# Kernel tuning notes

Hardware: AMD Instinct MI355X
Metric: run time of the kernel (lower is better)

The kernel has to match this reference:

```python
import jax, jax.numpy as jnp
import numpy as np

PAGE_SIZE = 16
NUM_PAGES = 256
H = 32          # query heads
HKV = 8         # kv heads
D = 128         # head dim
HIDDEN = 4096
SEQ = 2048
ROPE_THETA = 10000.0


def _rope(x, pos):
    # x: [S, h, D], pos: [S]; non-interleaved (rotate-half) RoPE as in
    # flashinfer.rope.apply_rope_pos_ids_inplace / HF Llama.
    half = x.shape[-1] // 2
    inv_freq = 1.0 / (ROPE_THETA ** (jnp.arange(half, dtype=jnp.float32) / half))
    ang = pos.astype(jnp.float32)[:, None] * inv_freq          # [S, half]
    cos = jnp.cos(ang)[:, None, :]
    sin = jnp.sin(ang)[:, None, :]
    x1, x2 = x[..., :half], x[..., half:]
    return jnp.concatenate([x1 * cos - x2 * sin, x2 * cos + x1 * sin], axis=-1).astype(x.dtype)


def setup_inputs() -> dict:
    key = jax.random.key(0)
    ks = jax.random.split(key, 6)
    return {
        "hidden_states": jax.random.normal(ks[0], (1, SEQ, HIDDEN), jnp.float32),
        "position_ids": jnp.arange(SEQ, dtype=jnp.int32),
        "page_indices": jnp.arange(SEQ // PAGE_SIZE, dtype=jnp.int32),  # 128 distinct pages
        "Wq": jax.random.normal(ks[1], (H * D, HIDDEN), jnp.float32) * 0.02,
        "Wk": jax.random.normal(ks[2], (HKV * D, HIDDEN), jnp.float32) * 0.02,
        "Wv": jax.random.normal(ks[3], (HKV * D, HIDDEN), jnp.float32) * 0.02,
        "Wo": jax.random.normal(ks[4], (HIDDEN, H * D), jnp.float32) * 0.02,
        "kv_cache": jnp.zeros((NUM_PAGES, 2, PAGE_SIZE, HKV, D), jnp.float32),
    }


def reference(hidden_states, position_ids, page_indices, Wq, Wk, Wv, Wo, kv_cache):
    S = hidden_states.shape[1]
    x = hidden_states[0]                                  # [S, HIDDEN] (module squeezes batch=1)
    q = (x @ Wq.T).reshape(S, H, D)
    k = (x @ Wk.T).reshape(S, HKV, D)
    v = (x @ Wv.T).reshape(S, HKV, D)
    q = _rope(q, position_ids)
    k = _rope(k, position_ids)

    # Write K/V into the paged cache (page_table.write_block per page)
    n_used = page_indices.shape[0]
    k_pages = k.reshape(n_used, PAGE_SIZE, HKV, D)
    v_pages = v.reshape(n_used, PAGE_SIZE, HKV, D)
    cache = kv_cache.at[page_indices, 0].set(k_pages).at[page_indices, 1].set(v_pages)

    # Gather paged KV back for attention (BatchPrefillWithPagedKVCache)
    kk = cache[page_indices, 0].reshape(-1, HKV, D)[:S]   # [S, HKV, D]
    vv = cache[page_indices, 1].reshape(-1, HKV, D)[:S]

    # GQA: expand kv heads to query heads
    group = H // HKV
    k_rep = jnp.repeat(kk, group, axis=1)                 # [S, H, D]
    v_rep = jnp.repeat(vv, group, axis=1)

    scale = D ** -0.5
    scores = jnp.einsum('qhd,khd->hqk', q * scale, k_rep)  # [H, S, S]
    causal = jnp.arange(S)[:, None] >= jnp.arange(S)[None, :]
    scores = jnp.where(causal[None], scores, jnp.finfo(scores.dtype).min)
    probs = jax.nn.softmax(scores, axis=-1)
    attn = jnp.einsum('hqk,khd->qhd', probs, v_rep)        # [S, H, D]

    out = attn.reshape(S, H * D) @ Wo.T                    # o_proj
    return out[None]                                       # [1, S, HIDDEN]
```

## Files before the change

kernel.cpp:

```cpp
#include <hip/hip_runtime.h>
#include <hip/hip_bf16.h>
#include <math.h>

#define SEQ    2048
#define HIDDEN 4096
#define NH     32
#define NKV    8
#define HD     128
#define QKV_N  6144

typedef __attribute__((ext_vector_type(8))) short bf16x8;
typedef __attribute__((ext_vector_type(4))) float f32x4;
typedef unsigned short u16;
typedef unsigned int u32;

#define VMCNT(n) asm volatile("s_waitcnt vmcnt(" #n ")" ::: "memory")

__device__ inline void gl_lds16(const void* g, void* lds) {
  __builtin_amdgcn_global_load_lds((const __attribute__((address_space(1))) void*)g,
                                   (__attribute__((address_space(3))) void*)lds, 16, 0, 0);
}

__device__ inline void tile_barrier() {
  __builtin_amdgcn_sched_barrier(0);
  __builtin_amdgcn_s_barrier();
  __builtin_amdgcn_sched_barrier(0);
}

__device__ inline u16 f2bf(float f) {
  __hip_bfloat16 h = __float2bfloat16(f);
  return *(u16*)&h;
}
__device__ inline float bf2f(u16 u) {
  __hip_bfloat16 h = *(__hip_bfloat16*)&u;
  return __bfloat162float(h);
}

__global__ void cvt_f32_bf16(const float* __restrict__ src, u16* __restrict__ dst, int n8) {
  int i = blockIdx.x * blockDim.x + threadIdx.x;
  if (i >= n8) return;
  const float4* s = (const float4*)src + (size_t)i * 2;
  float4 a = s[0], b = s[1];
  float v[8] = {a.x, a.y, a.z, a.w, b.x, b.y, b.z, b.w};
  union { u16 o[8]; uint4 u; } pk;
#pragma unroll
  for (int j = 0; j < 8; j++) pk.o[j] = f2bf(v[j]);
  *(uint4*)(dst + (size_t)i * 8) = pk.u;
}

template <int OUTF32, int NF>
__global__ __launch_bounds__(512, 2) void gemm_bt2(const u16* __restrict__ A,
                                                   const u16* __restrict__ B,
                                                   void* __restrict__ Cout,
                                                   int M, int N, int K) {
  __shared__ __align__(16) u16 Abuf[4][256 * 32];
  __shared__ __align__(16) u16 Bbuf[4][NF * 64 * 32];
  const int tid = threadIdx.x;
  const int w = tid >> 6, lane = tid & 63;
  const int quad = lane >> 4, l16 = lane & 15;
  const int wm = w >> 2, wn = w & 3;
  constexpr int BN = NF * 64;

  const int nwg = gridDim.x;
  const int bid = blockIdx.x;
  const int qq = nwg >> 3, rr8 = nwg & 7;
  const int xcd = bid & 7, loc = bid >> 3;
  const int wg = (xcd < rr8 ? xcd * (qq + 1) : rr8 * (qq + 1) + (xcd - rr8) * qq) + loc;
  const int nbx = N / BN;
  const int m0 = (wg / nbx) * 256;
  const int n0 = (wg % nbx) * BN;

  const int srow = lane >> 2;
  const int sswz = ((lane >> 2) & 3) ^ ((lane >> 4) & 1);
  const int scol = ((lane & 3) ^ sswz) << 3;
  const u16* aG = A + (size_t)(m0 + w * 16 + srow) * K + scol;
  const u16* bG = B + (size_t)(n0 + w * 16 + srow) * K + scol;
  const int NT = K >> 5;

  const int swzr = (l16 & 3) ^ ((l16 >> 2) & 1);
  const int kslot = (quad ^ swzr) << 3;

  f32x4 acc[8][NF] = {};

  auto stage = [&](int t) {
    const int b = t & 3;
    const size_t k0 = (size_t)t << 5;
    gl_lds16(aG + k0,                   &Abuf[b][(w * 16) * 32]);
    gl_lds16(aG + k0 + (size_t)128 * K, &Abuf[b][(128 + w * 16) * 32]);
    gl_lds16(bG + k0,                   &Bbuf[b][(w * 16) * 32]);
    if constexpr (NF == 4)
      gl_lds16(bG + k0 + (size_t)128 * K, &Bbuf[b][(128 + w * 16) * 32]);
  };

  stage(0); stage(1); stage(2);
  if constexpr (NF == 4) { VMCNT(8); } else { VMCNT(6); }
  tile_barrier();

  for (int t = 0; t < NT; ++t) {
    const int b = t & 3;
    if (t + 3 < NT) stage(t + 3);

    bf16x8 af[8], bfr[NF];
#pragma unroll
    for (int f = 0; f < 8; ++f)
      af[f] = *(const bf16x8*)&Abuf[b][(wm * 128 + f * 16 + l16) * 32 + kslot];
#pragma unroll
    for (int nf = 0; nf < NF; ++nf)
      bfr[nf] = *(const bf16x8*)&Bbuf[b][(wn * (NF * 16) + nf * 16 + l16) * 32 + kslot];

    __builtin_amdgcn_s_setprio(1);
#pragma unroll
    for (int f = 0; f < 8; ++f)
#pragma unroll
      for (int nf = 0; nf < NF; ++nf)
        acc[f][nf] = __builtin_amdgcn_mfma_f32_16x16x32_bf16(af[f], bfr[nf], acc[f][nf], 0, 0, 0);
    __builtin_amdgcn_s_setprio(0);

    if (t < NT - 1) {
      if (t + 3 < NT) {
        if constexpr (NF == 4) { VMCNT(8); } else { VMCNT(6); }
      } else if (t + 3 == NT) {
        if constexpr (NF == 4) { VMCNT(4); } else { VMCNT(3); }
      } else {
        VMCNT(0);
      }
      tile_barrier();
    }
  }

#pragma unroll
  for (int f = 0; f < 8; ++f)
#pragma unroll
    for (int nf = 0; nf < NF; ++nf)
#pragma unroll
      for (int r = 0; r < 4; ++r) {
        int row = m0 + wm * 128 + f * 16 + quad * 4 + r;
        int col = n0 + wn * (NF * 16) + nf * 16 + l16;
        float v = acc[f][nf][r];
        if (OUTF32) ((float*)Cout)[(size_t)row * N + col] = v;
        else        ((u16*)Cout)[(size_t)row * N + col] = f2bf(v);
      }
}

__global__ void rope_kernel(u16* __restrict__ qkv, const int* __restrict__ pos_ids) {
  int idx = blockIdx.x * blockDim.x + threadIdx.x;
  int d = idx & 63;
  int h = (idx >> 6) % 40;
  int s = idx / (64 * 40);
  if (s >= SEQ) return;
  int off = (h < NH) ? h * HD : HIDDEN + (h - NH) * HD;
  u16* base = qkv + (size_t)s * QKV_N + off;
  float inv_freq = powf(10000.0f, -(float)d * (1.0f / 64.0f));
  float ang = (float)pos_ids[s] * inv_freq;
  float sn, cs;
  sincosf(ang, &sn, &cs);
  float x1 = bf2f(base[d]);
  float x2 = bf2f(base[d + 64]);
  base[d]      = f2bf(x1 * cs - x2 * sn);
  base[d + 64] = f2bf(x2 * cs + x1 * sn);
}

__global__ __launch_bounds__(256) void transpose_v(const u16* __restrict__ qkv,
                                                   u16* __restrict__ vt) {
  __shared__ u16 t[64][72];
  const int s0 = blockIdx.x * 64, c0 = blockIdx.y * 64;
  const int tid = threadIdx.x;
#pragma unroll
  for (int i = 0; i < 2; i++) {
    int r = (tid >> 3) + i * 32;
    int c = (tid & 7) * 8;
    *(uint4*)&t[r][c] = *(const uint4*)&qkv[(size_t)(s0 + r) * QKV_N + 5120 + c0 + c];
  }
  __syncthreads();
#pragma unroll
  for (int i = 0; i < 2; i++) {
    int c = (tid >> 3) + i * 32;
    int s = (tid & 7) * 8;
    union { uint4 u; u16 e[8]; } o;
#pragma unroll
    for (int j = 0; j < 8; j++) o.e[j] = t[s + j][c];
    *(uint4*)&vt[(size_t)(c0 + c) * SEQ + s0 + s] = o.u;
  }
}

__global__ __launch_bounds__(128, 3) void attn_kernel(const u16* __restrict__ qkv,
                                                      const u16* __restrict__ vt,
                                                      u16* __restrict__ attn_out) {
  __shared__ __align__(16) float Ex[32 * 132];
  const int blk = blockIdx.x;
  const int kvh = blk & 7;
  const int hg = (blk >> 3) & 3;
  const int it = 63 - (blk >> 5);
  const int h  = kvh * 4 + hg;
  const int tid = threadIdx.x;
  const int wave = tid >> 6, lane = tid & 63;
  const int quad = lane >> 4, l16 = lane & 15;
  const int q0 = it * 32;

  const float c = 0.08838834764831845f * 1.4426950408889634f;

  bf16x8 qf[2][4];
#pragma unroll
  for (int m = 0; m < 2; m++)
#pragma unroll
    for (int dc = 0; dc < 4; dc++)
      qf[m][dc] = *(const bf16x8*)(qkv + (size_t)(q0 + m * 16 + l16) * QKV_N + h * HD + dc * 32 + quad * 8);

  const u16* kp[4];
#pragma unroll
  for (int st = 0; st < 4; st++)
    kp[st] = qkv + (size_t)(wave * 64 + st * 16 + l16) * QKV_N + HIDDEN + kvh * HD + quad * 8;
  const u16* vp[8];
#pragma unroll
  for (int dt = 0; dt < 8; dt++)
    vp[dt] = vt + (size_t)(kvh * HD + dt * 16 + l16) * SEQ + wave * 64 + quad * 8;

  float lsum[2] = {0.f, 0.f};
  f32x4 o[2][8] = {};

  const int srcA = ((lane >> 4) & 1) * 32 + l16;
  const int srcB = srcA + 16;
  const bool hi = quad >= 2;

  const int n_kt = (q0 + 95) >> 6;
  for (int kt = wave; kt < n_kt; kt += 2) {
    const bool last = (kt == n_kt - 1);

    u32 pk[2][4][2];
#pragma unroll
    for (int st = 0; st < 4; st++) {
      bf16x8 kst[4];
#pragma unroll
      for (int dc = 0; dc < 4; dc++) kst[dc] = *(const bf16x8*)(kp[st] + dc * 32);
      f32x4 s[2] = {};
#pragma unroll
      for (int dc = 0; dc < 4; dc++)
#pragma unroll
        for (int m = 0; m < 2; m++)
          s[m] = __builtin_amdgcn_mfma_f32_16x16x32_bf16(kst[dc], qf[m][dc], s[m], 0, 0, 0);
#pragma unroll
      for (int m = 0; m < 2; m++) {
        float pr[4];
#pragma unroll
        for (int r = 0; r < 4; r++) {
          float v = fmaf(s[m][r], c, -32.0f);
          if (last) {
            int key = kt * 64 + st * 16 + quad * 4 + r;
            if (key > q0 + m * 16 + l16) v = -1e30f;
          }
          pr[r] = exp2f(v);
          lsum[m] += pr[r];
        }
        pk[m][st][0] = ((u32)f2bf(pr[1]) << 16) | f2bf(pr[0]);
        pk[m][st][1] = ((u32)f2bf(pr[3]) << 16) | f2bf(pr[2]);
      }
    }

    bf16x8 pf[2][2];
#pragma unroll
    for (int m = 0; m < 2; m++)
#pragma unroll
      for (int kc = 0; kc < 2; kc++) {
        union { u32 w[4]; bf16x8 v; } u;
        u32 a0 = (u32)__shfl((int)pk[m][2 * kc][0],     srcA);
        u32 b0 = (u32)__shfl((int)pk[m][2 * kc + 1][0], srcA);
        u32 a1 = (u32)__shfl((int)pk[m][2 * kc][1],     srcA);
        u32 b1 = (u32)__shfl((int)pk[m][2 * kc + 1][1], srcA);
        u32 a2 = (u32)__shfl((int)pk[m][2 * kc][0],     srcB);
        u32 b2 = (u32)__shfl((int)pk[m][2 * kc + 1][0], srcB);
        u32 a3 = (u32)__shfl((int)pk[m][2 * kc][1],     srcB);
        u32 b3 = (u32)__shfl((int)pk[m][2 * kc + 1][1], srcB);
        u.w[0] = hi ? b0 : a0;
        u.w[1] = hi ? b1 : a1;
        u.w[2] = hi ? b2 : a2;
        u.w[3] = hi ? b3 : a3;
        pf[m][kc] = u.v;
      }

#pragma unroll
    for (int dt = 0; dt < 8; dt++) {
      bf16x8 vf0 = *(const bf16x8*)(vp[dt]);
      bf16x8 vf1 = *(const bf16x8*)(vp[dt] + 32);
#pragma unroll
      for (int m = 0; m < 2; m++) {
        o[m][dt] = __builtin_amdgcn_mfma_f32_16x16x32_bf16(vf0, pf[m][0], o[m][dt], 0, 0, 0);
        o[m][dt] = __builtin_amdgcn_mfma_f32_16x16x32_bf16(vf1, pf[m][1], o[m][dt], 0, 0, 0);
      }
    }

#pragma unroll
    for (int st = 0; st < 4; st++) kp[st] += (size_t)128 * QKV_N;
#pragma unroll
    for (int dt = 0; dt < 8; dt++) vp[dt] += 128;
  }

#pragma unroll
  for (int m = 0; m < 2; m++) {
    lsum[m] += __shfl_xor(lsum[m], 16);
    lsum[m] += __shfl_xor(lsum[m], 32);
  }

  if (wave == 1) {
#pragma unroll
    for (int m = 0; m < 2; m++) {
#pragma unroll
      for (int dt = 0; dt < 8; dt++)
        *(f32x4*)&Ex[(m * 16 + l16) * 132 + dt * 16 + quad * 4] = o[m][dt];
      if (lane < 16) Ex[(m * 16 + l16) * 132 + 128] = lsum[m];
    }
  }
  __syncthreads();
  if (wave == 0) {
#pragma unroll
    for (int m = 0; m < 2; m++) {
      float lt = lsum[m] + Ex[(m * 16 + l16) * 132 + 128];
      float inv = 1.0f / lt;
      size_t base = (size_t)(q0 + m * 16 + l16) * HIDDEN + h * HD;
#pragma unroll
      for (int dt = 0; dt < 8; dt++) {
        f32x4 p = *(const f32x4*)&Ex[(m * 16 + l16) * 132 + dt * 16 + quad * 4];
        float v0 = (o[m][dt][0] + p[0]) * inv;
        float v1 = (o[m][dt][1] + p[1]) * inv;
        float v2 = (o[m][dt][2] + p[2]) * inv;
        float v3 = (o[m][dt][3] + p[3]) * inv;
        u32 w0 = ((u32)f2bf(v1) << 16) | f2bf(v0);
        u32 w1 = ((u32)f2bf(v3) << 16) | f2bf(v2);
        uint2 wv; wv.x = w0; wv.y = w1;
        *(uint2*)&attn_out[base + dt * 16 + quad * 4] = wv;
      }
    }
  }
}

extern "C" void kernel_launch(void* const* d_in, const int* in_sizes, int n_in,
                              void* d_out, int out_size, void* d_ws, size_t ws_size,
                              hipStream_t stream) {
  const float* x  = (const float*)d_in[0];
  const int* pos  = (const int*)d_in[1];
  const float* Wq = (const float*)d_in[3];
  const float* Wk = (const float*)d_in[4];
  const float* Wv = (const float*)d_in[5];
  const float* Wo = (const float*)d_in[6];
  float* out = (float*)d_out;

  u16* x_bf    = (u16*)d_ws;
  u16* Wqkv_bf = x_bf + (size_t)SEQ * HIDDEN;
  u16* qkv_bf  = Wqkv_bf + (size_t)QKV_N * HIDDEN;
  u16* attn_bf = qkv_bf + (size_t)SEQ * QKV_N;
  u16* Wo_bf   = attn_bf + (size_t)SEQ * HIDDEN;
  u16* vt_bf   = x_bf;

  auto cvt = [&](const float* s, u16* d, size_t n) {
    int n8 = (int)(n / 8);
    cvt_f32_bf16<<<(n8 + 255) / 256, 256, 0, stream>>>(s, d, n8);
  };
  cvt(x,  x_bf,    (size_t)SEQ * HIDDEN);
  cvt(Wq, Wqkv_bf,                         (size_t)4096 * 4096);
  cvt(Wk, Wqkv_bf + (size_t)4096 * 4096,   (size_t)1024 * 4096);
  cvt(Wv, Wqkv_bf + (size_t)5120 * 4096,   (size_t)1024 * 4096);
  cvt(Wo, Wo_bf,   (size_t)4096 * 4096);

  gemm_bt2<0, 4><<<dim3((SEQ / 256) * (QKV_N / 256)), 512, 0, stream>>>(
      x_bf, Wqkv_bf, qkv_bf, SEQ, QKV_N, HIDDEN);

  int rope_threads = SEQ * 40 * 64;
  rope_kernel<<<rope_threads / 256, 256, 0, stream>>>(qkv_bf, pos);

  dim3 gt(SEQ / 64, 1024 / 64);
  transpose_v<<<gt, 256, 0, stream>>>(qkv_bf, vt_bf);

  attn_kernel<<<2048, 128, 0, stream>>>(qkv_bf, vt_bf, attn_bf);

  gemm_bt2<1, 2><<<dim3((SEQ / 256) * (HIDDEN / 128)), 512, 0, stream>>>(
      attn_bf, Wo_bf, out, SEQ, HIDDEN, HIDDEN);
}
```

Before: 700.2 us.

## Retile GEMMs with 192-wide QKV tiles and split-phase staged pipeline

Replaces the GEMM kernel with one that splits each K-step into two half-M MFMA phases. The A and B prefetches are interleaved between those phases with extra barriers. The QKV projection now uses 256x192 tiles, so 256 workgroups fill the CUs instead of 192, and tiles are mapped per XCD along N. The output projection uses a 3-deep ring with higher occupancy. The LDS XOR swizzle is dropped, which risks LDS bank conflicts on fragment reads, and the added barriers add synchronization cost.

```diff
diff --git a/kernel.cpp b/kernel.cpp
--- a/kernel.cpp
+++ b/kernel.cpp
@@ -15,13 +15,15 @@
 typedef unsigned int u32;
 
 #define VMCNT(n) asm volatile("s_waitcnt vmcnt(" #n ")" ::: "memory")
+#define LGKM0 do { asm volatile("s_waitcnt lgkmcnt(0)" ::: "memory"); \
+                   __builtin_amdgcn_sched_barrier(0); } while (0)
 
 __device__ inline void gl_lds16(const void* g, void* lds) {
   __builtin_amdgcn_global_load_lds((const __attribute__((address_space(1))) void*)g,
                                    (__attribute__((address_space(3))) void*)lds, 16, 0, 0);
 }
 
-__device__ inline void tile_barrier() {
+__device__ inline void tile_bar() {
   __builtin_amdgcn_sched_barrier(0);
   __builtin_amdgcn_s_barrier();
   __builtin_amdgcn_sched_barrier(0);
@@ -49,94 +51,120 @@
 }
 
 template <int OUTF32, int NF>
-__global__ __launch_bounds__(512, 2) void gemm_bt2(const u16* __restrict__ A,
-                                                   const u16* __restrict__ B,
-                                                   void* __restrict__ Cout,
-                                                   int M, int N, int K) {
-  __shared__ __align__(16) u16 Abuf[4][256 * 32];
-  __shared__ __align__(16) u16 Bbuf[4][NF * 64 * 32];
+__global__ __launch_bounds__(512, NF == 2 ? 4 : 2)
+void gemm8p(const u16* __restrict__ A, const u16* __restrict__ B,
+            void* __restrict__ Cout, int M, int N, int K) {
+  constexpr int RING  = (NF == 2) ? 3 : 4;
+  constexpr int BROWS = (NF == 2) ? 128 : 256;
+  constexpr int A_ELE = 256 * 32;
+  constexpr int B_ELE = BROWS * 32;
+  __shared__ __align__(16) u16 Ab[RING * A_ELE];
+  __shared__ __align__(16) u16 Bb[RING * B_ELE];
+
   const int tid = threadIdx.x;
   const int w = tid >> 6, lane = tid & 63;
   const int quad = lane >> 4, l16 = lane & 15;
   const int wm = w >> 2, wn = w & 3;
   constexpr int BN = NF * 64;
 
-  const int nwg = gridDim.x;
   const int bid = blockIdx.x;
-  const int qq = nwg >> 3, rr8 = nwg & 7;
-  const int xcd = bid & 7, loc = bid >> 3;
-  const int wg = (xcd < rr8 ? xcd * (qq + 1) : rr8 * (qq + 1) + (xcd - rr8) * qq) + loc;
-  const int nbx = N / BN;
-  const int m0 = (wg / nbx) * 256;
-  const int n0 = (wg % nbx) * BN;
-
-  const int srow = lane >> 2;
-  const int sswz = ((lane >> 2) & 3) ^ ((lane >> 4) & 1);
-  const int scol = ((lane & 3) ^ sswz) << 3;
-  const u16* aG = A + (size_t)(m0 + w * 16 + srow) * K + scol;
-  const u16* bG = B + (size_t)(n0 + w * 16 + srow) * K + scol;
+  const int nbn = N / BN;
+  const int npx = nbn >> 3;
+  const int n_idx = (bid & 7) * npx + ((bid >> 3) % npx);
+  const int m_idx = bid / (8 * npx);
+  const int m0 = m_idx * 256, n0 = n_idx * BN;
+
+  const u16* aS = A + (size_t)(m0 + w * 16 + (lane >> 2)) * K + (lane & 3) * 8;
+  const u16* bS = B + (size_t)(n0 + w * 16 + (lane >> 2)) * K + (lane & 3) * 8;
+  const size_t boff2 = (size_t)((NF == 3 && w >= 4) ? 0 : 128) * K;
+
   const int NT = K >> 5;
 
-  const int swzr = (l16 & 3) ^ ((l16 >> 2) & 1);
-  const int kslot = (quad ^ swzr) << 3;
-
   f32x4 acc[8][NF] = {};
 
-  auto stage = [&](int t) {
-    const int b = t & 3;
-    const size_t k0 = (size_t)t << 5;
-    gl_lds16(aG + k0,                   &Abuf[b][(w * 16) * 32]);
-    gl_lds16(aG + k0 + (size_t)128 * K, &Abuf[b][(128 + w * 16) * 32]);
-    gl_lds16(bG + k0,                   &Bbuf[b][(w * 16) * 32]);
+  auto stageA = [&](int t) {
+    const int b = t % RING;
+    gl_lds16(aS + (size_t)t * 32, &Ab[b * A_ELE + (w * 16) * 32]);
+    gl_lds16(aS + (size_t)128 * K + (size_t)t * 32, &Ab[b * A_ELE + (128 + w * 16) * 32]);
+  };
+  auto stageB = [&](int t) {
+    const int b = t % RING;
+    gl_lds16(bS + (size_t)t * 32, &Bb[b * B_ELE + (w * 16) * 32]);
+    if constexpr (NF == 3)
+      gl_lds16(bS + boff2 + (size_t)t * 32, &Bb[b * B_ELE + (128 + w * 16) * 32]);
     if constexpr (NF == 4)
-      gl_lds16(bG + k0 + (size_t)128 * K, &Bbuf[b][(128 + w * 16) * 32]);
+      gl_lds16(bS + (size_t)128 * K + (size_t)t * 32, &Bb[b * B_ELE + (128 + w * 16) * 32]);
   };
 
-  stage(0); stage(1); stage(2);
-  if constexpr (NF == 4) { VMCNT(8); } else { VMCNT(6); }
-  tile_barrier();
+  if constexpr (NF == 2) {
+    stageA(0); stageB(0); stageA(1); stageB(1);
+    VMCNT(3);
+  } else {
+    stageA(0); stageB(0); stageA(1); stageB(1); stageA(2); stageB(2);
+    VMCNT(8);
+  }
+  tile_bar();
 
   for (int t = 0; t < NT; ++t) {
-    const int b = t & 3;
-    if (t + 3 < NT) stage(t + 3);
-
-    bf16x8 af[8], bfr[NF];
-#pragma unroll
-    for (int f = 0; f < 8; ++f)
-      af[f] = *(const bf16x8*)&Abuf[b][(wm * 128 + f * 16 + l16) * 32 + kslot];
-#pragma unroll
-    for (int nf = 0; nf < NF; ++nf)
-      bfr[nf] = *(const bf16x8*)&Bbuf[b][(wn * (NF * 16) + nf * 16 + l16) * 32 + kslot];
-
+    const int b = t % RING;
+    const u16* Abt = &Ab[b * A_ELE];
+    const u16* Bbt = &Bb[b * B_ELE];
+
+    bf16x8 af0[4], bfv[NF];
+#pragma unroll
+    for (int f = 0; f < 4; ++f)
+      af0[f] = *(const bf16x8*)&Abt[(wm * 128 + f * 16 + l16) * 32 + quad * 8];
+#pragma unroll
+    for (int n = 0; n < NF; ++n)
+      bfv[n] = *(const bf16x8*)&Bbt[(wn * (NF * 16) + n * 16 + l16) * 32 + quad * 8];
+    if (t + RING - 1 < NT) stageA(t + RING - 1);
+    tile_bar();
+    LGKM0;
     __builtin_amdgcn_s_setprio(1);
 #pragma unroll
-    for (int f = 0; f < 8; ++f)
-#pragma unroll
-      for (int nf = 0; nf < NF; ++nf)
-        acc[f][nf] = __builtin_amdgcn_mfma_f32_16x16x32_bf16(af[f], bfr[nf], acc[f][nf], 0, 0, 0);
+    for (int f = 0; f < 4; ++f)
+#pragma unroll
+      for (int n = 0; n < NF; ++n)
+        acc[f][n] = __builtin_amdgcn_mfma_f32_16x16x32_bf16(af0[f], bfv[n], acc[f][n], 0, 0, 0);
     __builtin_amdgcn_s_setprio(0);
+    tile_bar();
+
+    bf16x8 af1[4];
+#pragma unroll
+    for (int f = 0; f < 4; ++f)
+      af1[f] = *(const bf16x8*)&Abt[(wm * 128 + (4 + f) * 16 + l16) * 32 + quad * 8];
+    if (t + RING - 1 < NT) stageB(t + RING - 1);
+    tile_bar();
+    LGKM0;
+    __builtin_amdgcn_s_setprio(1);
+#pragma unroll
+    for (int f = 0; f < 4; ++f)
+#pragma unroll
+      for (int n = 0; n < NF; ++n)
+        acc[4 + f][n] = __builtin_amdgcn_mfma_f32_16x16x32_bf16(af1[f], bfv[n], acc[4 + f][n], 0, 0, 0);
+    __builtin_amdgcn_s_setprio(0);
 
     if (t < NT - 1) {
-      if (t + 3 < NT) {
-        if constexpr (NF == 4) { VMCNT(8); } else { VMCNT(6); }
-      } else if (t + 3 == NT) {
-        if constexpr (NF == 4) { VMCNT(4); } else { VMCNT(3); }
+      if constexpr (NF == 2) {
+        if (t + 2 < NT) { VMCNT(3); } else { VMCNT(0); }
       } else {
-        VMCNT(0);
-      }
-      tile_barrier();
+        if (t + 3 < NT)       { VMCNT(8); }
+        else if (t + 3 == NT) { VMCNT(4); }
+        else                  { VMCNT(0); }
+      }
+      tile_bar();
     }
   }
 
 #pragma unroll
   for (int f = 0; f < 8; ++f)
 #pragma unroll
-    for (int nf = 0; nf < NF; ++nf)
+    for (int n = 0; n < NF; ++n)
 #pragma unroll
       for (int r = 0; r < 4; ++r) {
         int row = m0 + wm * 128 + f * 16 + quad * 4 + r;
-        int col = n0 + wn * (NF * 16) + nf * 16 + l16;
-        float v = acc[f][nf][r];
+        int col = n0 + wn * (NF * 16) + n * 16 + l16;
+        float v = acc[f][n][r];
         if (OUTF32) ((float*)Cout)[(size_t)row * N + col] = v;
         else        ((u16*)Cout)[(size_t)row * N + col] = f2bf(v);
       }
@@ -360,8 +388,7 @@
   cvt(Wv, Wqkv_bf + (size_t)5120 * 4096,   (size_t)1024 * 4096);
   cvt(Wo, Wo_bf,   (size_t)4096 * 4096);
 
-  gemm_bt2<0, 4><<<dim3((SEQ / 256) * (QKV_N / 256)), 512, 0, stream>>>(
-      x_bf, Wqkv_bf, qkv_bf, SEQ, QKV_N, HIDDEN);
+  gemm8p<0, 3><<<dim3(256), 512, 0, stream>>>(x_bf, Wqkv_bf, qkv_bf, SEQ, QKV_N, HIDDEN);
 
   int rope_threads = SEQ * 40 * 64;
   rope_kernel<<<rope_threads / 256, 256, 0, stream>>>(qkv_bf, pos);
@@ -371,6 +398,5 @@
 
   attn_kernel<<<2048, 128, 0, stream>>>(qkv_bf, vt_bf, attn_bf);
 
-  gemm_bt2<1, 2><<<dim3((SEQ / 256) * (HIDDEN / 128)), 512, 0, stream>>>(
-      attn_bf, Wo_bf, out, SEQ, HIDDEN, HIDDEN);
-}
+  gemm8p<1, 2><<<dim3(256), 512, 0, stream>>>(attn_bf, Wo_bf, out, SEQ, HIDDEN, HIDDEN);
+}
```

Result: faster. 629.9 us (-10.0%).
